# Performance work log

Hardware: AMD Instinct MI355X
Metric: run time of the kernel (lower is better)

Reference implementation:

```python
import jax, jax.numpy as jnp
import numpy as np

N_HEADS = 32
KV_HEADS = 8
HEAD_DIM = 64
THETA = 10000.0


def _rope_tables(L, head_dim, dtype):
    freqs = 1.0 / (THETA ** (jnp.arange(0, head_dim, 2, dtype=jnp.float32) / head_dim))
    phases = jnp.outer(jnp.arange(L, dtype=jnp.float32), freqs)  # [L, head_dim//2]
    phases = jnp.concatenate([phases, phases], axis=-1)          # [L, head_dim]
    return jnp.cos(phases).astype(dtype), jnp.sin(phases).astype(dtype)


def _rotate_half(x):
    x1, x2 = jnp.split(x, 2, axis=-1)
    return jnp.concatenate([-x2, x1], axis=-1)


def setup_inputs() -> dict:
    key = jax.random.key(0)
    ks = jax.random.split(key, 5)
    B, L, D = 2, 2048, 2048
    kv_dim = KV_HEADS * HEAD_DIM
    s = 0.02
    return {
        "x": jax.random.normal(ks[0], (B, L, D), jnp.float32),
        "wq": jax.random.normal(ks[1], (D, D), jnp.float32) * s,
        "wk": jax.random.normal(ks[2], (kv_dim, D), jnp.float32) * s,
        "wv": jax.random.normal(ks[3], (kv_dim, D), jnp.float32) * s,
        "wo": jax.random.normal(ks[4], (D, D), jnp.float32) * s,
    }


def reference(x, wq, wk, wv, wo):
    B, L, D = x.shape
    rep = N_HEADS // KV_HEADS
    cos, sin = _rope_tables(L, HEAD_DIM, x.dtype)  # [L, hd]

    # projections (torch Linear: y = x @ W.T)
    q = jnp.einsum('bld,ed->ble', x, wq).reshape(B, L, N_HEADS, HEAD_DIM).transpose(0, 2, 1, 3)   # [B,H,L,hd]
    k = jnp.einsum('bld,ed->ble', x, wk).reshape(B, L, KV_HEADS, HEAD_DIM).transpose(0, 2, 1, 3)  # [B,Hk,L,hd]
    v = jnp.einsum('bld,ed->ble', x, wv).reshape(B, L, KV_HEADS, HEAD_DIM).transpose(0, 2, 1, 3)

    # RoPE (broadcast over batch/heads)
    q = cos * q + _rotate_half(q) * sin
    k = cos * k + _rotate_half(k) * sin

    # GQA attention without materializing repeated K/V: group query heads per kv head
    qg = q.reshape(B, KV_HEADS, rep, L, HEAD_DIM)
    scale = 1.0 / jnp.sqrt(jnp.asarray(HEAD_DIM, x.dtype))
    scores = jnp.einsum('bkrqd,bkld->bkrql', qg, k) * scale  # [B,Hk,rep,L,L]
    causal = jnp.tril(jnp.ones((L, L), bool))
    scores = jnp.where(causal, scores, jnp.asarray(-jnp.inf, scores.dtype))
    attn = jax.nn.softmax(scores, axis=-1)
    out = jnp.einsum('bkrql,bkld->bkrqd', attn, v)           # [B,Hk,rep,L,hd]
    out = out.reshape(B, N_HEADS, L, HEAD_DIM).transpose(0, 2, 1, 3).reshape(B, L, D)
    return jnp.einsum('ble,de->bld', out, wo)
```

## Files before the change

### kernel.cpp

```cpp
#include <hip/hip_runtime.h>

typedef __attribute__((ext_vector_type(8))) __bf16 bf16x8;
typedef __attribute__((ext_vector_type(8))) ushort u16x8;
typedef __attribute__((ext_vector_type(4))) float f32x4;
typedef __attribute__((ext_vector_type(16))) float f32x16;

#define MFMA16(a, b, c) __builtin_amdgcn_mfma_f32_16x16x32_bf16(a, b, c, 0, 0, 0)
#define MFMA32(a, b, c) __builtin_amdgcn_mfma_f32_32x32x16_bf16(a, b, c, 0, 0, 0)

__device__ __forceinline__ ushort f2bf(float f) {
    union { float f; unsigned u; } v; v.f = f;
    unsigned r = v.u + 0x7FFFu + ((v.u >> 16) & 1u);
    return (ushort)(r >> 16);
}
__device__ __forceinline__ float bf2f(ushort b) {
    union { unsigned u; float f; } v; v.u = ((unsigned)b) << 16; return v.f;
}
__device__ __forceinline__ int cvtpk(float lo, float hi) {
    int r; asm("v_cvt_pk_bf16_f32 %0, %1, %2" : "=v"(r) : "v"(lo), "v"(hi)); return r;
}
__device__ __forceinline__ float fexp2(float x) {
    float r; asm("v_exp_f32 %0, %1" : "=v"(r) : "v"(x)); return r;
}
__device__ __forceinline__ void gload_lds16(const void* g, void* l) {
    __builtin_amdgcn_global_load_lds((const __attribute__((address_space(1))) void*)g,
                                     (__attribute__((address_space(3))) void*)l, 16, 0, 0);
}

__device__ __forceinline__ int swz8(int row, int g) {
    return row * 64 + (((g) ^ (row & 7)) << 3);
}
__device__ __forceinline__ int swz16(int row, int g) {
    return row * 128 + (((g) ^ (row & 15)) << 3);
}

__device__ __forceinline__ void stage64(const ushort* __restrict__ g, int rs,
                                        char* lds, int tid) {
    const int r = tid >> 3;
    const int c8 = ((tid & 7) ^ (r & 7)) << 3;
    const int wid = tid >> 6;
    gload_lds16(g + (size_t)r * rs + c8, lds + wid * 1024);
    gload_lds16(g + (size_t)(r + 32) * rs + c8, lds + 4096 + wid * 1024);
}

__device__ __forceinline__ void stageV128(const ushort* __restrict__ g, char* lds, int tid) {
    const int w = tid >> 6, l = tid & 63;
    const int g16 = l & 15;
#pragma unroll
    for (int j = 0; j < 4; ++j) {
        const int r = w * 16 + j * 4 + (l >> 4);
        gload_lds16(g + (size_t)r * 2048 + ((g16 ^ (r & 15)) << 3), lds + w * 4096 + j * 1024);
    }
}

__global__ void cvt_all(const float* __restrict__ x,  const float* __restrict__ wq,
                        const float* __restrict__ wk, const float* __restrict__ wv,
                        const float* __restrict__ wo, ushort* __restrict__ xb,
                        ushort* __restrict__ wcat, ushort* __restrict__ wob,
                        float* __restrict__ cosT, float* __restrict__ sinT) {
    int i = blockIdx.x * 256 + threadIdx.x;
    if (i >= 4718592) {
        int id = i - 4718592;
        if (id < 65536) {
            int fi = id >> 11, l = id & 2047;
            float freq = __expf(-(float)fi * (9.210340371976184f / 32.0f));
            float ph = (float)l * freq;
            cosT[id] = cosf(ph);
            sinT[id] = sinf(ph);
        }
        return;
    }
    const float* src; ushort* dst; int off;
    if (i < 2097152)      { src = x;  dst = xb;             off = i; }
    else if (i < 3145728) { src = wq; dst = wcat;           off = i - 2097152; }
    else if (i < 3407872) { src = wk; dst = wcat + 4194304; off = i - 3145728; }
    else if (i < 3670016) { src = wv; dst = wcat + 5242880; off = i - 3407872; }
    else                  { src = wo; dst = wob;            off = i - 3670016; }
    float4 v = ((const float4*)src)[off];
    ushort4 o;
    o.x = f2bf(v.x); o.y = f2bf(v.y); o.z = f2bf(v.z); o.w = f2bf(v.w);
    ((ushort4*)dst)[off] = o;
}

template <int EPI, int BN, int WM, int WN>
__global__ __launch_bounds__(512, 2) void gemmK(const ushort* __restrict__ A,
                                                const ushort* __restrict__ B,
                                                void* __restrict__ Cp,
                                                ushort* __restrict__ vt,
                                                const float* __restrict__ cosT,
                                                const float* __restrict__ sinT,
                                                int M, int N, int K) {
    constexpr int MF = 256 / WM / 16;
    constexpr int NF = BN / WN / 16;
    constexpr int BLOADS = BN / 128;
    constexpr int TLOADS = 2 + BLOADS;
    constexpr int ABUF = 256 * 32;
    constexpr int BBUF = BN * 32;
    extern __shared__ __align__(16) ushort sm[];
    ushort* sA = sm;
    ushort* sB = sm + 3 * ABUF;
    const int tid = threadIdx.x, lane = tid & 63, wid = tid >> 6;
    const int wr = wid / WN, wc = wid % WN;
    const int lr = lane & 15, lg = lane >> 4;
    const int m0 = blockIdx.y * 256, n0 = blockIdx.x * BN;
    const int NT = K >> 5;
    const int csrc = ((tid & 3) ^ ((tid >> 3) & 3)) << 3;
    const int co = ((lg ^ ((lr >> 1) & 3)) << 3);
    const ushort* gAt = A + (size_t)(m0 + (tid >> 2)) * K + csrc;
    const ushort* gBt = B + (size_t)(n0 + (tid >> 2)) * K + csrc;

    auto stgA = [&](int t, int buf) {
        const ushort* g = gAt + t * 32;
        char* ld = (char*)(sA + buf * ABUF) + wid * 1024;
        gload_lds16(g, ld);
        gload_lds16(g + (size_t)128 * K, ld + 8192);
    };
    auto stgB = [&](int t, int buf) {
        const ushort* g = gBt + t * 32;
        char* ld = (char*)(sB + buf * BBUF) + wid * 1024;
        gload_lds16(g, ld);
        if constexpr (BLOADS == 2) gload_lds16(g + (size_t)128 * K, ld + 8192);
    };

    f32x4 acc[MF][NF] = {};
    stgA(0, 0); stgB(0, 0); stgA(1, 1); stgB(1, 1);
    if constexpr (TLOADS == 4) asm volatile("s_waitcnt vmcnt(4)" ::: "memory");
    else                       asm volatile("s_waitcnt vmcnt(3)" ::: "memory");
    __builtin_amdgcn_s_barrier();

    int cur = 0, stg = 2;
    for (int t = 0; t < NT; ++t) {
        const ushort* Ac = sA + cur * ABUF + (wr * (256 / WM)) * 32 + co;
        const ushort* Bc = sB + cur * BBUF + (wc * (BN / WN)) * 32 + co;
        if constexpr (BN == 256) {
            bf16x8 bfr[NF], af[MF / 2];
#pragma unroll
            for (int nf = 0; nf < NF; ++nf) bfr[nf] = *(const bf16x8*)&Bc[(nf * 16 + lr) * 32];
#pragma unroll
            for (int mf = 0; mf < MF / 2; ++mf) af[mf] = *(const bf16x8*)&Ac[(mf * 16 + lr) * 32];
            if (t + 2 < NT) stgA(t + 2, stg);
            __builtin_amdgcn_s_barrier();
            __builtin_amdgcn_s_setprio(1);
#pragma unroll
            for (int mf = 0; mf < MF / 2; ++mf)
#pragma unroll
                for (int nf = 0; nf < NF; ++nf)
                    acc[mf][nf] = MFMA16(af[mf], bfr[nf], acc[mf][nf]);
            __builtin_amdgcn_s_setprio(0);
            __builtin_amdgcn_s_barrier();
            bf16x8 af2[MF - MF / 2];
#pragma unroll
            for (int mf = 0; mf < MF - MF / 2; ++mf)
                af2[mf] = *(const bf16x8*)&Ac[((mf + MF / 2) * 16 + lr) * 32];
            if (t + 2 < NT) {
                stgB(t + 2, stg);
                asm volatile("s_waitcnt vmcnt(4)" ::: "memory");
            } else {
                asm volatile("s_waitcnt vmcnt(0)" ::: "memory");
            }
            __builtin_amdgcn_s_barrier();
            __builtin_amdgcn_s_setprio(1);
#pragma unroll
            for (int mf = 0; mf < MF - MF / 2; ++mf)
#pragma unroll
                for (int nf = 0; nf < NF; ++nf)
                    acc[mf + MF / 2][nf] = MFMA16(af2[mf], bfr[nf], acc[mf + MF / 2][nf]);
            __builtin_amdgcn_s_setprio(0);
            __builtin_amdgcn_s_barrier();
        } else {
            bf16x8 bfr[NF], af[MF];
#pragma unroll
            for (int nf = 0; nf < NF; ++nf) bfr[nf] = *(const bf16x8*)&Bc[(nf * 16 + lr) * 32];
#pragma unroll
            for (int mf = 0; mf < MF; ++mf) af[mf] = *(const bf16x8*)&Ac[(mf * 16 + lr) * 32];
            if (t + 2 < NT) {
                stgA(t + 2, stg); stgB(t + 2, stg);
                asm volatile("s_waitcnt vmcnt(3)" ::: "memory");
            } else {
                asm volatile("s_waitcnt vmcnt(0)" ::: "memory");
            }
            __builtin_amdgcn_s_barrier();
            __builtin_amdgcn_s_setprio(1);
#pragma unroll
            for (int mf = 0; mf < MF; ++mf)
#pragma unroll
                for (int nf = 0; nf < NF; ++nf)
                    acc[mf][nf] = MFMA16(af[mf], bfr[nf], acc[mf][nf]);
            __builtin_amdgcn_s_setprio(0);
            __builtin_amdgcn_s_barrier();
        }
        cur = (cur == 2) ? 0 : cur + 1;
        stg = (stg == 2) ? 0 : stg + 1;
    }

    const int r0 = m0 + wr * (256 / WM) + lg * 4;
    const int c0 = n0 + wc * (BN / WN) + lr;
    if constexpr (EPI == 1) {
        float* C = (float*)Cp;
#pragma unroll
        for (int mi = 0; mi < MF; ++mi)
#pragma unroll
            for (int ni = 0; ni < NF; ++ni)
#pragma unroll
                for (int r = 0; r < 4; ++r)
                    C[(size_t)(r0 + mi * 16 + r) * N + c0 + ni * 16] = acc[mi][ni][r];
    } else {
        const int wavecol = n0 + wc * (BN / WN);
        ushort* qkv = (ushort*)Cp;
        if (wavecol >= 2560) {
            const int kh = (wavecol - 2560) >> 6;
            const int b = m0 >> 11;
            const int l0 = r0 & 2047;
#pragma unroll
            for (int ni = 0; ni < NF; ++ni) {
                const int d = lr + ni * 16;
                ushort* vrow = vt + (size_t)((b * 8 + kh) * 64 + d) * 2048 + l0;
#pragma unroll
                for (int mi = 0; mi < MF; ++mi) {
                    ushort4 o;
                    o.x = f2bf(acc[mi][ni][0]); o.y = f2bf(acc[mi][ni][1]);
                    o.z = f2bf(acc[mi][ni][2]); o.w = f2bf(acc[mi][ni][3]);
                    *(ushort4*)(vrow + mi * 16) = o;
                }
            }
        } else {
            const float scale = (wavecol < 2048) ? 0.18033688f : 1.0f;
            const int l0 = r0 & 2047;
#pragma unroll
            for (int ni = 0; ni < NF / 2; ++ni) {
                const int i = ni * 16 + lr;
                const float* cp = cosT + i * 2048 + l0;
                const float* sp = sinT + i * 2048 + l0;
#pragma unroll
                for (int mi = 0; mi < MF; ++mi) {
                    float4 cv = *(const float4*)(cp + mi * 16);
                    float4 sv = *(const float4*)(sp + mi * 16);
#pragma unroll
                    for (int r = 0; r < 4; ++r) {
                        float lo = acc[mi][ni][r], hi = acc[mi][ni + 2][r];
                        float c = ((const float*)&cv)[r], s = ((const float*)&sv)[r];
                        size_t row = (size_t)(r0 + mi * 16 + r) * 3072;
                        qkv[row + c0 + ni * 16]      = f2bf((c * lo - s * hi) * scale);
                        qkv[row + c0 + ni * 16 + 32] = f2bf((c * hi + s * lo) * scale);
                    }
                }
            }
        }
    }
}

__global__ __launch_bounds__(256, 2) void attn_k(const ushort* __restrict__ qkv,
                                                 const ushort* __restrict__ vt,
                                                 ushort* __restrict__ attn) {
    extern __shared__ __align__(16) ushort smem[];
    const int tid = threadIdx.x, lane = tid & 63, wid = tid >> 6;
    const int hl = lane >> 5, lq = lane & 31;
    const int p = blockIdx.x;
    const int head = blockIdx.y, b = blockIdx.z;
    const int kh = head >> 2;

    const ushort* Kg = qkv + (size_t)(b * 2048) * 3072 + 2048 + kh * 64;
    const ushort* Vg = vt + (size_t)((b * 8 + kh) * 64) * 2048;

    for (int ph = 0; ph < 2; ++ph) {
        const int qt = ph ? p : 15 - p;
        const int qb = qt << 7;
        const int qw0 = qb + wid * 32;
        const int q_lane = qw0 + lq;
        const int nt = qt + 1;

        bf16x8 qf[4];
        {
            const ushort* qp = qkv + (size_t)(b * 2048 + qw0 + lq) * 3072 + head * 64 + hl * 8;
#pragma unroll
            for (int j = 0; j < 4; ++j) qf[j] = *(const bf16x8*)(qp + j * 16);
        }
        f32x16 o0 = {}, o1 = {};
        float lsum = 0.f;

        stage64(Kg, 3072, (char*)smem, tid);
        stage64(Kg + (size_t)64 * 3072, 3072, (char*)smem + 8192, tid);
        stageV128(Vg, (char*)(smem + 16384), tid);

        for (int it = 0; it < nt; ++it) {
            const int c = it & 1;
            const int kv0 = it << 7;
            const ushort* Kc = smem + c * 8192;
            const ushort* Vc = smem + 16384 + c * 8192;
            if (it + 1 < nt) {
                const int kv1 = kv0 + 128;
                char* kd = (char*)smem + (c ^ 1) * 16384;
                char* vd = (char*)(smem + 16384) + (c ^ 1) * 16384;
                stage64(Kg + (size_t)kv1 * 3072, 3072, kd, tid);
                stage64(Kg + (size_t)(kv1 + 64) * 3072, 3072, kd + 8192, tid);
                stageV128(Vg + kv1, vd, tid);
                asm volatile("s_waitcnt vmcnt(8)" ::: "memory");
            } else {
                asm volatile("s_waitcnt vmcnt(0)" ::: "memory");
            }
            __builtin_amdgcn_s_barrier();

            f32x16 s0 = {}, s1 = {}, s2 = {}, s3 = {};
            __builtin_amdgcn_s_setprio(1);
#pragma unroll
            for (int j = 0; j < 4; ++j) {
                bf16x8 k0 = *(const bf16x8*)&Kc[swz8(lq, j * 2 + hl)];
                bf16x8 k1 = *(const bf16x8*)&Kc[swz8(32 + lq, j * 2 + hl)];
                bf16x8 k2 = *(const bf16x8*)&Kc[swz8(64 + lq, j * 2 + hl)];
                bf16x8 k3 = *(const bf16x8*)&Kc[swz8(96 + lq, j * 2 + hl)];
                s0 = MFMA32(k0, qf[j], s0);
                s1 = MFMA32(k1, qf[j], s1);
                s2 = MFMA32(k2, qf[j], s2);
                s3 = MFMA32(k3, qf[j], s3);
            }
            __builtin_amdgcn_s_setprio(0);

            if (it == qt) {
#pragma unroll
                for (int i = 0; i < 16; ++i) {
                    int r = (i & 3) + ((i >> 2) << 3) + (hl << 2) + kv0;
                    if (r > q_lane)      s0[i] = -1e30f;
                    if (r + 32 > q_lane) s1[i] = -1e30f;
                    if (r + 64 > q_lane) s2[i] = -1e30f;
                    if (r + 96 > q_lane) s3[i] = -1e30f;
                }
            }
#pragma unroll
            for (int i = 0; i < 16; ++i) s0[i] = fexp2(s0[i]);
#pragma unroll
            for (int i = 0; i < 16; ++i) s1[i] = fexp2(s1[i]);
#pragma unroll
            for (int i = 0; i < 16; ++i) s2[i] = fexp2(s2[i]);
#pragma unroll
            for (int i = 0; i < 16; ++i) s3[i] = fexp2(s3[i]);
            f32x16 ts = (s0 + s1) + (s2 + s3);
            float u0 = ts[0] + ts[1], u1 = ts[2] + ts[3], u2 = ts[4] + ts[5], u3 = ts[6] + ts[7];
            float u4 = ts[8] + ts[9], u5 = ts[10] + ts[11], u6 = ts[12] + ts[13], u7 = ts[14] + ts[15];
            float rs = ((u0 + u1) + (u2 + u3)) + ((u4 + u5) + (u6 + u7));
            {
                auto sw = __builtin_amdgcn_permlane32_swap(__float_as_int(rs), __float_as_int(rs), 0, 0);
                rs = __int_as_float(sw[0]) + __int_as_float(sw[1]);
            }
            lsum += rs;

            bf16x8 pf[8];
#define PFB(cc, q0, q1, q2, q3, q4, q5, q6, q7)                                   \
            {                                                                      \
                int pk01 = cvtpk(q0, q1), pk23 = cvtpk(q2, q3);                    \
                int pk45 = cvtpk(q4, q5), pk67 = cvtpk(q6, q7);                    \
                auto sA = __builtin_amdgcn_permlane32_swap(pk01, pk45, 0, 0);      \
                auto sB = __builtin_amdgcn_permlane32_swap(pk23, pk67, 0, 0);      \
                union { int w[4]; bf16x8 v; } u;                                   \
                u.w[0] = sA[0]; u.w[1] = sB[0]; u.w[2] = sA[1]; u.w[3] = sB[1];    \
                pf[cc] = u.v;                                                      \
            }
            PFB(0, s0[0], s0[1], s0[2], s0[3], s0[4], s0[5], s0[6], s0[7])
            PFB(1, s0[8], s0[9], s0[10], s0[11], s0[12], s0[13], s0[14], s0[15])
            PFB(2, s1[0], s1[1], s1[2], s1[3], s1[4], s1[5], s1[6], s1[7])
            PFB(3, s1[8], s1[9], s1[10], s1[11], s1[12], s1[13], s1[14], s1[15])
            PFB(4, s2[0], s2[1], s2[2], s2[3], s2[4], s2[5], s2[6], s2[7])
            PFB(5, s2[8], s2[9], s2[10], s2[11], s2[12], s2[13], s2[14], s2[15])
            PFB(6, s3[0], s3[1], s3[2], s3[3], s3[4], s3[5], s3[6], s3[7])
            PFB(7, s3[8], s3[9], s3[10], s3[11], s3[12], s3[13], s3[14], s3[15])
#undef PFB
            __builtin_amdgcn_s_setprio(1);
#pragma unroll
            for (int cc = 0; cc < 8; ++cc) {
                bf16x8 v0 = *(const bf16x8*)&Vc[swz16(lq, cc * 2 + hl)];
                bf16x8 v1 = *(const bf16x8*)&Vc[swz16(32 + lq, cc * 2 + hl)];
                o0 = MFMA32(v0, pf[cc], o0);
                o1 = MFMA32(v1, pf[cc], o1);
            }
            __builtin_amdgcn_s_setprio(0);
            __builtin_amdgcn_s_barrier();
        }

        __syncthreads();
        ushort* sc = (ushort*)((char*)smem + wid * 4096);
        float inv = 1.0f / lsum;
#pragma unroll
        for (int i = 0; i < 16; i += 2) {
            int d0 = (i & 3) + ((i >> 2) << 3) + (hl << 2);
            int g0 = d0 >> 3, g1 = (d0 + 32) >> 3;
            *(int*)&sc[lq * 64 + ((g0 ^ (lq & 7)) << 3) + (d0 & 7)] = cvtpk(o0[i] * inv, o0[i + 1] * inv);
            *(int*)&sc[lq * 64 + ((g1 ^ (lq & 7)) << 3) + (d0 & 7)] = cvtpk(o1[i] * inv, o1[i + 1] * inv);
        }
        __syncthreads();
        {
            const int q = lane >> 1, db = (lane & 1) << 5;
            const size_t orow = (size_t)(b * 2048 + qb + wid * 32 + q);
#pragma unroll
            for (int j = 0; j < 4; ++j) {
                int g = (db >> 3) + j;
                u16x8 v = *(const u16x8*)&sc[q * 64 + ((g ^ (q & 7)) << 3)];
                *(u16x8*)(attn + orow * 2048 + head * 64 + g * 8) = v;
            }
        }
        __syncthreads();
    }
}

extern "C" void kernel_launch(void* const* d_in, const int* in_sizes, int n_in,
                              void* d_out, int out_size, void* d_ws, size_t ws_size,
                              hipStream_t stream) {
    const float* x  = (const float*)d_in[0];
    const float* wq = (const float*)d_in[1];
    const float* wk = (const float*)d_in[2];
    const float* wv = (const float*)d_in[3];
    const float* wo = (const float*)d_in[4];
    float* out = (float*)d_out;
    char* ws = (char*)d_ws;

    ushort* xb   = (ushort*)(ws);
    ushort* wcat = (ushort*)(ws + 16777216);
    ushort* wob  = (ushort*)(ws + 29360128);
    ushort* qkv  = (ushort*)(ws + 37748736);
    ushort* vt   = (ushort*)(ws + 62914560);
    ushort* attn = (ushort*)(ws + 67108864);
    float*  cosT = (float*)(ws + 83886080);
    float*  sinT = (float*)(ws + 84148224);

    (void)hipFuncSetAttribute((const void*)gemmK<2, 256, 2, 4>,
                              hipFuncAttributeMaxDynamicSharedMemorySize, 98304);
    (void)hipFuncSetAttribute((const void*)gemmK<1, 128, 4, 2>,
                              hipFuncAttributeMaxDynamicSharedMemorySize, 73728);
    (void)hipFuncSetAttribute((const void*)attn_k,
                              hipFuncAttributeMaxDynamicSharedMemorySize, 65536);

    cvt_all<<<18688, 256, 0, stream>>>(x, wq, wk, wv, wo, xb, wcat, wob, cosT, sinT);
    gemmK<2, 256, 2, 4><<<dim3(12, 16), 512, 98304, stream>>>(xb, wcat, qkv, vt, cosT, sinT,
                                                              4096, 3072, 2048);
    attn_k<<<dim3(8, 32, 2), 256, 65536, stream>>>(qkv, vt, attn);
    gemmK<1, 128, 4, 2><<<dim3(16, 16), 512, 73728, stream>>>(attn, wob, out, nullptr, nullptr,
                                                              nullptr, 4096, 2048, 2048);
}
```

Before: 175.3 us.

## Split GEMM template; add K=64 double-buffered output GEMM and XCD-aware block swizzle

Specializes the QKV projection GEMM into its own kernel and replaces the output projection GEMM with a new kernel. The new kernel uses a K-step of 64, double buffering and an 8-way XOR-swizzled LDS layout, and does one barrier pair per step. Both GEMMs now launch a 1D grid, with the block index remapped so consecutive tiles spread across XCDs for better L2 locality. The aim is to halve loop and barrier overhead in the output projection and improve cache reuse, at the cost of more LDS per block and a shallower prefetch depth.

```diff
diff --git a/kernel.cpp b/kernel.cpp
--- a/kernel.cpp
+++ b/kernel.cpp
@@ -82,27 +82,24 @@
     ((ushort4*)dst)[off] = o;
 }
 
-template <int EPI, int BN, int WM, int WN>
-__global__ __launch_bounds__(512, 2) void gemmK(const ushort* __restrict__ A,
-                                                const ushort* __restrict__ B,
-                                                void* __restrict__ Cp,
-                                                ushort* __restrict__ vt,
-                                                const float* __restrict__ cosT,
-                                                const float* __restrict__ sinT,
-                                                int M, int N, int K) {
-    constexpr int MF = 256 / WM / 16;
-    constexpr int NF = BN / WN / 16;
-    constexpr int BLOADS = BN / 128;
-    constexpr int TLOADS = 2 + BLOADS;
-    constexpr int ABUF = 256 * 32;
-    constexpr int BBUF = BN * 32;
+__global__ __launch_bounds__(512, 2) void gemmQKV(const ushort* __restrict__ A,
+                                                  const ushort* __restrict__ B,
+                                                  ushort* __restrict__ qkv,
+                                                  ushort* __restrict__ vt,
+                                                  const float* __restrict__ cosT,
+                                                  const float* __restrict__ sinT,
+                                                  int M, int N, int K, int gx) {
+    constexpr int MF = 8, NF = 4;
+    constexpr int ABUF = 256 * 32, BBUF = 256 * 32;
     extern __shared__ __align__(16) ushort sm[];
     ushort* sA = sm;
     ushort* sB = sm + 3 * ABUF;
     const int tid = threadIdx.x, lane = tid & 63, wid = tid >> 6;
-    const int wr = wid / WN, wc = wid % WN;
+    const int wr = wid >> 2, wc = wid & 3;
     const int lr = lane & 15, lg = lane >> 4;
-    const int m0 = blockIdx.y * 256, n0 = blockIdx.x * BN;
+    const int nwg = gridDim.x, bid = blockIdx.x;
+    const int swz = (bid & 7) * (nwg >> 3) + (bid >> 3);
+    const int m0 = (swz / gx) * 256, n0 = (swz % gx) * 256;
     const int NT = K >> 5;
     const int csrc = ((tid & 3) ^ ((tid >> 3) & 3)) << 3;
     const int co = ((lg ^ ((lr >> 1) & 3)) << 3);
@@ -119,134 +116,182 @@
         const ushort* g = gBt + t * 32;
         char* ld = (char*)(sB + buf * BBUF) + wid * 1024;
         gload_lds16(g, ld);
-        if constexpr (BLOADS == 2) gload_lds16(g + (size_t)128 * K, ld + 8192);
+        gload_lds16(g + (size_t)128 * K, ld + 8192);
     };
 
     f32x4 acc[MF][NF] = {};
     stgA(0, 0); stgB(0, 0); stgA(1, 1); stgB(1, 1);
-    if constexpr (TLOADS == 4) asm volatile("s_waitcnt vmcnt(4)" ::: "memory");
-    else                       asm volatile("s_waitcnt vmcnt(3)" ::: "memory");
+    asm volatile("s_waitcnt vmcnt(4)" ::: "memory");
     __builtin_amdgcn_s_barrier();
 
     int cur = 0, stg = 2;
     for (int t = 0; t < NT; ++t) {
-        const ushort* Ac = sA + cur * ABUF + (wr * (256 / WM)) * 32 + co;
-        const ushort* Bc = sB + cur * BBUF + (wc * (BN / WN)) * 32 + co;
-        if constexpr (BN == 256) {
-            bf16x8 bfr[NF], af[MF / 2];
-#pragma unroll
-            for (int nf = 0; nf < NF; ++nf) bfr[nf] = *(const bf16x8*)&Bc[(nf * 16 + lr) * 32];
-#pragma unroll
-            for (int mf = 0; mf < MF / 2; ++mf) af[mf] = *(const bf16x8*)&Ac[(mf * 16 + lr) * 32];
-            if (t + 2 < NT) stgA(t + 2, stg);
-            __builtin_amdgcn_s_barrier();
-            __builtin_amdgcn_s_setprio(1);
-#pragma unroll
-            for (int mf = 0; mf < MF / 2; ++mf)
-#pragma unroll
-                for (int nf = 0; nf < NF; ++nf)
-                    acc[mf][nf] = MFMA16(af[mf], bfr[nf], acc[mf][nf]);
-            __builtin_amdgcn_s_setprio(0);
-            __builtin_amdgcn_s_barrier();
-            bf16x8 af2[MF - MF / 2];
-#pragma unroll
-            for (int mf = 0; mf < MF - MF / 2; ++mf)
-                af2[mf] = *(const bf16x8*)&Ac[((mf + MF / 2) * 16 + lr) * 32];
-            if (t + 2 < NT) {
-                stgB(t + 2, stg);
-                asm volatile("s_waitcnt vmcnt(4)" ::: "memory");
-            } else {
-                asm volatile("s_waitcnt vmcnt(0)" ::: "memory");
-            }
-            __builtin_amdgcn_s_barrier();
-            __builtin_amdgcn_s_setprio(1);
-#pragma unroll
-            for (int mf = 0; mf < MF - MF / 2; ++mf)
-#pragma unroll
-                for (int nf = 0; nf < NF; ++nf)
-                    acc[mf + MF / 2][nf] = MFMA16(af2[mf], bfr[nf], acc[mf + MF / 2][nf]);
-            __builtin_amdgcn_s_setprio(0);
-            __builtin_amdgcn_s_barrier();
+        const ushort* Ac = sA + cur * ABUF + (wr * 128) * 32 + co;
+        const ushort* Bc = sB + cur * BBUF + (wc * 64) * 32 + co;
+        bf16x8 bfr[NF], af[MF / 2];
+#pragma unroll
+        for (int nf = 0; nf < NF; ++nf) bfr[nf] = *(const bf16x8*)&Bc[(nf * 16 + lr) * 32];
+#pragma unroll
+        for (int mf = 0; mf < MF / 2; ++mf) af[mf] = *(const bf16x8*)&Ac[(mf * 16 + lr) * 32];
+        if (t + 2 < NT) stgA(t + 2, stg);
+        __builtin_amdgcn_s_barrier();
+        __builtin_amdgcn_s_setprio(1);
+#pragma unroll
+        for (int mf = 0; mf < MF / 2; ++mf)
+#pragma unroll
+            for (int nf = 0; nf < NF; ++nf)
+                acc[mf][nf] = MFMA16(af[mf], bfr[nf], acc[mf][nf]);
+        __builtin_amdgcn_s_setprio(0);
+        __builtin_amdgcn_s_barrier();
+        bf16x8 af2[MF / 2];
+#pragma unroll
+        for (int mf = 0; mf < MF / 2; ++mf)
+            af2[mf] = *(const bf16x8*)&Ac[((mf + MF / 2) * 16 + lr) * 32];
+        if (t + 2 < NT) {
+            stgB(t + 2, stg);
+            asm volatile("s_waitcnt vmcnt(4)" ::: "memory");
         } else {
-            bf16x8 bfr[NF], af[MF];
-#pragma unroll
-            for (int nf = 0; nf < NF; ++nf) bfr[nf] = *(const bf16x8*)&Bc[(nf * 16 + lr) * 32];
-#pragma unroll
-            for (int mf = 0; mf < MF; ++mf) af[mf] = *(const bf16x8*)&Ac[(mf * 16 + lr) * 32];
-            if (t + 2 < NT) {
-                stgA(t + 2, stg); stgB(t + 2, stg);
-                asm volatile("s_waitcnt vmcnt(3)" ::: "memory");
-            } else {
-                asm volatile("s_waitcnt vmcnt(0)" ::: "memory");
-            }
-            __builtin_amdgcn_s_barrier();
-            __builtin_amdgcn_s_setprio(1);
-#pragma unroll
-            for (int mf = 0; mf < MF; ++mf)
-#pragma unroll
-                for (int nf = 0; nf < NF; ++nf)
-                    acc[mf][nf] = MFMA16(af[mf], bfr[nf], acc[mf][nf]);
-            __builtin_amdgcn_s_setprio(0);
-            __builtin_amdgcn_s_barrier();
-        }
+            asm volatile("s_waitcnt vmcnt(0)" ::: "memory");
+        }
+        __builtin_amdgcn_s_barrier();
+        __builtin_amdgcn_s_setprio(1);
+#pragma unroll
+        for (int mf = 0; mf < MF / 2; ++mf)
+#pragma unroll
+            for (int nf = 0; nf < NF; ++nf)
+                acc[mf + MF / 2][nf] = MFMA16(af2[mf], bfr[nf], acc[mf + MF / 2][nf]);
+        __builtin_amdgcn_s_setprio(0);
+        __builtin_amdgcn_s_barrier();
         cur = (cur == 2) ? 0 : cur + 1;
         stg = (stg == 2) ? 0 : stg + 1;
     }
 
-    const int r0 = m0 + wr * (256 / WM) + lg * 4;
-    const int c0 = n0 + wc * (BN / WN) + lr;
-    if constexpr (EPI == 1) {
-        float* C = (float*)Cp;
-#pragma unroll
-        for (int mi = 0; mi < MF; ++mi)
-#pragma unroll
-            for (int ni = 0; ni < NF; ++ni)
-#pragma unroll
-                for (int r = 0; r < 4; ++r)
-                    C[(size_t)(r0 + mi * 16 + r) * N + c0 + ni * 16] = acc[mi][ni][r];
+    const int r0 = m0 + wr * 128 + lg * 4;
+    const int c0 = n0 + wc * 64 + lr;
+    const int wavecol = n0 + wc * 64;
+    if (wavecol >= 2560) {
+        const int kh = (wavecol - 2560) >> 6;
+        const int b = m0 >> 11;
+        const int l0 = r0 & 2047;
+#pragma unroll
+        for (int ni = 0; ni < NF; ++ni) {
+            const int d = lr + ni * 16;
+            ushort* vrow = vt + (size_t)((b * 8 + kh) * 64 + d) * 2048 + l0;
+#pragma unroll
+            for (int mi = 0; mi < MF; ++mi) {
+                ushort4 o;
+                o.x = f2bf(acc[mi][ni][0]); o.y = f2bf(acc[mi][ni][1]);
+                o.z = f2bf(acc[mi][ni][2]); o.w = f2bf(acc[mi][ni][3]);
+                *(ushort4*)(vrow + mi * 16) = o;
+            }
+        }
     } else {
-        const int wavecol = n0 + wc * (BN / WN);
-        ushort* qkv = (ushort*)Cp;
-        if (wavecol >= 2560) {
-            const int kh = (wavecol - 2560) >> 6;
-            const int b = m0 >> 11;
-            const int l0 = r0 & 2047;
-#pragma unroll
-            for (int ni = 0; ni < NF; ++ni) {
-                const int d = lr + ni * 16;
-                ushort* vrow = vt + (size_t)((b * 8 + kh) * 64 + d) * 2048 + l0;
-#pragma unroll
-                for (int mi = 0; mi < MF; ++mi) {
-                    ushort4 o;
-                    o.x = f2bf(acc[mi][ni][0]); o.y = f2bf(acc[mi][ni][1]);
-                    o.z = f2bf(acc[mi][ni][2]); o.w = f2bf(acc[mi][ni][3]);
-                    *(ushort4*)(vrow + mi * 16) = o;
+        const float scale = (wavecol < 2048) ? 0.18033688f : 1.0f;
+        const int l0 = r0 & 2047;
+#pragma unroll
+        for (int ni = 0; ni < NF / 2; ++ni) {
+            const int i = ni * 16 + lr;
+            const float* cp = cosT + i * 2048 + l0;
+            const float* sp = sinT + i * 2048 + l0;
+#pragma unroll
+            for (int mi = 0; mi < MF; ++mi) {
+                float4 cv = *(const float4*)(cp + mi * 16);
+                float4 sv = *(const float4*)(sp + mi * 16);
+#pragma unroll
+                for (int r = 0; r < 4; ++r) {
+                    float lo = acc[mi][ni][r], hi = acc[mi][ni + 2][r];
+                    float c = ((const float*)&cv)[r], s = ((const float*)&sv)[r];
+                    size_t row = (size_t)(r0 + mi * 16 + r) * 3072;
+                    qkv[row + c0 + ni * 16]      = f2bf((c * lo - s * hi) * scale);
+                    qkv[row + c0 + ni * 16 + 32] = f2bf((c * hi + s * lo) * scale);
                 }
             }
+        }
+    }
+}
+
+__global__ __launch_bounds__(512, 2) void gemm64(const ushort* __restrict__ A,
+                                                 const ushort* __restrict__ B,
+                                                 float* __restrict__ C,
+                                                 int M, int N, int K, int gx) {
+    extern __shared__ __align__(16) ushort sm[];
+    ushort* sA = sm;
+    ushort* sB = sm + 32768;
+    const int tid = threadIdx.x, lane = tid & 63, wid = tid >> 6;
+    const int wr = wid >> 1, wc = wid & 1;
+    const int lr = lane & 15, lg = lane >> 4;
+    const int nwg = gridDim.x, bid = blockIdx.x;
+    const int swz = (bid & 7) * (nwg >> 3) + (bid >> 3);
+    const int m0 = (swz / gx) * 256, n0 = (swz % gx) * 128;
+    const int NT = K >> 6;
+    const int sr = tid >> 3;
+    const int sc8 = ((tid & 7) ^ (sr & 7)) << 3;
+    const ushort* gAt = A + (size_t)(m0 + sr) * K + sc8;
+    const ushort* gBt = B + (size_t)(n0 + sr) * K + sc8;
+
+    auto stgA = [&](int t, int buf) {
+        const ushort* g = gAt + t * 64;
+        char* ld = (char*)(sA + buf * 16384) + wid * 1024;
+#pragma unroll
+        for (int s = 0; s < 4; ++s)
+            gload_lds16(g + (size_t)(s * 64) * K, ld + s * 8192);
+    };
+    auto stgB = [&](int t, int buf) {
+        const ushort* g = gBt + t * 64;
+        char* ld = (char*)(sB + buf * 8192) + wid * 1024;
+        gload_lds16(g, ld);
+        gload_lds16(g + (size_t)64 * K, ld + 8192);
+    };
+
+    f32x4 acc[4][4] = {};
+    stgA(0, 0); stgB(0, 0);
+    stgA(1, 1); stgB(1, 1);
+    asm volatile("s_waitcnt vmcnt(6)" ::: "memory");
+    __builtin_amdgcn_s_barrier();
+
+    for (int t = 0; t < NT; ++t) {
+        const int c = t & 1;
+        const ushort* Ac = sA + c * 16384 + (wr * 64) * 64;
+        const ushort* Bc = sB + c * 8192 + (wc * 64) * 64;
+        bf16x8 af[4][2], bfr[4][2];
+#pragma unroll
+        for (int mf = 0; mf < 4; ++mf)
+#pragma unroll
+            for (int kk = 0; kk < 2; ++kk)
+                af[mf][kk] = *(const bf16x8*)&Ac[swz8(mf * 16 + lr, kk * 4 + lg)];
+#pragma unroll
+        for (int nf = 0; nf < 4; ++nf)
+#pragma unroll
+            for (int kk = 0; kk < 2; ++kk)
+                bfr[nf][kk] = *(const bf16x8*)&Bc[swz8(nf * 16 + lr, kk * 4 + lg)];
+        __builtin_amdgcn_s_setprio(1);
+#pragma unroll
+        for (int mf = 0; mf < 4; ++mf)
+#pragma unroll
+            for (int nf = 0; nf < 4; ++nf)
+#pragma unroll
+                for (int kk = 0; kk < 2; ++kk)
+                    acc[mf][nf] = MFMA16(af[mf][kk], bfr[nf][kk], acc[mf][nf]);
+        __builtin_amdgcn_s_setprio(0);
+        __builtin_amdgcn_s_barrier();
+        if (t + 2 < NT) {
+            stgA(t + 2, c); stgB(t + 2, c);
+            asm volatile("s_waitcnt vmcnt(6)" ::: "memory");
         } else {
-            const float scale = (wavecol < 2048) ? 0.18033688f : 1.0f;
-            const int l0 = r0 & 2047;
-#pragma unroll
-            for (int ni = 0; ni < NF / 2; ++ni) {
-                const int i = ni * 16 + lr;
-                const float* cp = cosT + i * 2048 + l0;
-                const float* sp = sinT + i * 2048 + l0;
-#pragma unroll
-                for (int mi = 0; mi < MF; ++mi) {
-                    float4 cv = *(const float4*)(cp + mi * 16);
-                    float4 sv = *(const float4*)(sp + mi * 16);
-#pragma unroll
-                    for (int r = 0; r < 4; ++r) {
-                        float lo = acc[mi][ni][r], hi = acc[mi][ni + 2][r];
-                        float c = ((const float*)&cv)[r], s = ((const float*)&sv)[r];
-                        size_t row = (size_t)(r0 + mi * 16 + r) * 3072;
-                        qkv[row + c0 + ni * 16]      = f2bf((c * lo - s * hi) * scale);
-                        qkv[row + c0 + ni * 16 + 32] = f2bf((c * hi + s * lo) * scale);
-                    }
-                }
-            }
-        }
-    }
+            asm volatile("s_waitcnt vmcnt(0)" ::: "memory");
+        }
+        __builtin_amdgcn_s_barrier();
+    }
+
+    const int r0 = m0 + wr * 64 + lg * 4;
+    const int c0 = n0 + wc * 64 + lr;
+#pragma unroll
+    for (int mi = 0; mi < 4; ++mi)
+#pragma unroll
+        for (int ni = 0; ni < 4; ++ni)
+#pragma unroll
+            for (int r = 0; r < 4; ++r)
+                C[(size_t)(r0 + mi * 16 + r) * N + c0 + ni * 16] = acc[mi][ni][r];
 }
 
 __global__ __launch_bounds__(256, 2) void attn_k(const ushort* __restrict__ qkv,
@@ -420,17 +465,15 @@
     float*  cosT = (float*)(ws + 83886080);
     float*  sinT = (float*)(ws + 84148224);
 
-    (void)hipFuncSetAttribute((const void*)gemmK<2, 256, 2, 4>,
+    (void)hipFuncSetAttribute((const void*)gemmQKV,
                               hipFuncAttributeMaxDynamicSharedMemorySize, 98304);
-    (void)hipFuncSetAttribute((const void*)gemmK<1, 128, 4, 2>,
-                              hipFuncAttributeMaxDynamicSharedMemorySize, 73728);
+    (void)hipFuncSetAttribute((const void*)gemm64,
+                              hipFuncAttributeMaxDynamicSharedMemorySize, 98304);
     (void)hipFuncSetAttribute((const void*)attn_k,
                               hipFuncAttributeMaxDynamicSharedMemorySize, 65536);
 
     cvt_all<<<18688, 256, 0, stream>>>(x, wq, wk, wv, wo, xb, wcat, wob, cosT, sinT);
-    gemmK<2, 256, 2, 4><<<dim3(12, 16), 512, 98304, stream>>>(xb, wcat, qkv, vt, cosT, sinT,
-                                                              4096, 3072, 2048);
+    gemmQKV<<<192, 512, 98304, stream>>>(xb, wcat, qkv, vt, cosT, sinT, 4096, 3072, 2048, 12);
     attn_k<<<dim3(8, 32, 2), 256, 65536, stream>>>(qkv, vt, attn);
-    gemmK<1, 128, 4, 2><<<dim3(16, 16), 512, 73728, stream>>>(attn, wob, out, nullptr, nullptr,
-                                                              nullptr, 4096, 2048, 2048);
-}
+    gemm64<<<256, 512, 98304, stream>>>(attn, wob, out, 4096, 2048, 2048, 16);
+}
```

After: 172.4 us. No clear change (-1.7%).
